# Kernel optimization log

Hardware: AMD Instinct MI355X
Metric: run time of the kernel (lower is better)

## Reference

```python
import jax, jax.numpy as jnp
import numpy as np

B, N, C, H = 2, 2048, 128, 4
C4 = C // 4


def setup_inputs() -> dict:
    key = jax.random.key(0)
    ks = jax.random.split(key, 20)
    s = 0.02
    f = lambda k, sh: (jax.random.normal(k, sh, jnp.float32) * s)
    return {
        'x': jax.random.normal(ks[0], (B, N, C), jnp.float32),
        'A': jax.random.randint(ks[1], (N, N), 0, 2).astype(jnp.int32),
        'q_w1': f(ks[2], (C, C)), 'kv_w1': f(ks[3], (2 * C, C)),
        'proj_w1': f(ks[4], (C, C)), 'proj_b1': jnp.zeros((C,), jnp.float32),
        'q_w2': f(ks[5], (C, C)), 'kv_w2': f(ks[6], (2 * C, C)),
        'proj_w2': f(ks[7], (C, C)), 'proj_b2': jnp.zeros((C,), jnp.float32),
        'cq_w': f(ks[8], (C4, C)), 'cq_b': jnp.zeros((C4,), jnp.float32),
        'ck_w': f(ks[9], (C4, C)), 'ck_b': jnp.zeros((C4,), jnp.float32),
        'cv_w': f(ks[10], (C, C)), 'cv_b': jnp.zeros((C,), jnp.float32),
        'gc_w': f(ks[11], (C, C)), 'gc_b': jnp.zeros((C,), jnp.float32),
    }


def _attn_block(x, A, qw, kvw, pw, pb):
    # Attention._inner_attention + residual; qkv_bias=False, scale=head_dim**-0.5
    b, n, c = x.shape
    hd = c // H
    q = (x @ qw.T).reshape(b, n, H, hd).transpose(0, 2, 1, 3)          # [B,H,N,hd]
    kv = (x @ kvw.T).reshape(b, n, 2, H, hd).transpose(2, 0, 3, 1, 4)  # [2,B,H,N,hd]
    k, v = kv[0], kv[1]
    attn = jnp.einsum('bhnd,bhmd->bhnm', q, k) * (hd ** -0.5)
    attn = jnp.where(A[None, None] > 0, attn, jnp.float32(-9e15))
    attn = jax.nn.softmax(attn, axis=-1)
    out = jnp.einsum('bhnm,bhmd->bhnd', attn, v).transpose(0, 2, 1, 3).reshape(b, n, c)
    return out @ pw.T + pb + x


def _graph_conv(x, cq_w, cq_b, ck_w, ck_b, cv_w, cv_b, gc_w, gc_b):
    # GraphConvolution.forward: conv1d(k=1) QKV, softmax, topk scatter mask, masked softmax, bmm
    b, s, c = x.shape
    xp = x.transpose(0, 2, 1)                                          # [B,C,N]
    query = jnp.einsum('oi,bin->bon', cq_w, xp) + cq_b[:, None]        # [B,C/4,N]
    keyt = (jnp.einsum('oi,bin->bon', ck_w, xp) + ck_b[:, None]).transpose(0, 2, 1)  # [B,N,C/4]
    adj = jax.nn.softmax(jnp.einsum('bnc,bcm->bnm', keyt, query), axis=-1)           # [B,N,N]
    kk = int(s / 3 * 2)                                                # top-2/3 per row
    _, idx = jax.lax.top_k(adj, kk)                                    # [B,N,kk]
    mask = jnp.zeros(adj.shape, bool).at[
        jnp.arange(b)[:, None, None], jnp.arange(s)[None, :, None], idx].set(True)
    adj = jax.nn.softmax(jnp.where(mask, adj, -jnp.inf), axis=-1)
    value = (jnp.einsum('oi,bin->bon', cv_w, xp) + cv_b[:, None]).transpose(0, 2, 1)  # [B,N,C]
    support = value @ gc_w
    return jnp.einsum('bnm,bmc->bnc', adj, support) + gc_b


def reference(x, A, q_w1, kv_w1, proj_w1, proj_b1, q_w2, kv_w2, proj_w2, proj_b2,
              cq_w, cq_b, ck_w, ck_b, cv_w, cv_b, gc_w, gc_b):
    x = _attn_block(x, A, q_w1, kv_w1, proj_w1, proj_b1)
    x = _attn_block(x, A, q_w2, kv_w2, proj_w2, proj_b2)
    return _graph_conv(x, cq_w, cq_b, ck_w, ck_b, cv_w, cv_b, gc_w, gc_b)
```

## Files before the change

### kernel.cpp

```cpp
#include <hip/hip_runtime.h>
#include <hip/hip_bf16.h>
#include <math.h>

#define BB 2
#define NN 2048
#define CC 128
#define HH 4
#define HD 32
#define KK_TOP 1365

typedef __attribute__((ext_vector_type(8))) short v8s;
typedef __attribute__((ext_vector_type(4))) float f32x4;

#define MFMA16(a, b, c) __builtin_amdgcn_mfma_f32_16x16x32_bf16(a, b, c, 0, 0, 0)

__device__ inline float wave_max_f(float v) {
    #pragma unroll
    for (int m = 1; m < 64; m <<= 1) v = fmaxf(v, __shfl_xor(v, m));
    return v;
}
__device__ inline float wave_min_f(float v) {
    #pragma unroll
    for (int m = 1; m < 64; m <<= 1) v = fminf(v, __shfl_xor(v, m));
    return v;
}
__device__ inline float wave_sum_f(float v) {
    #pragma unroll
    for (int m = 1; m < 64; m <<= 1) v += __shfl_xor(v, m);
    return v;
}
__device__ inline unsigned short bf16bits(float x) {
    __hip_bfloat16 h = __float2bfloat16(x);
    return *reinterpret_cast<unsigned short*>(&h);
}

__global__ __launch_bounds__(256) void prep_k(
    const int* __restrict__ A, unsigned* __restrict__ Ab2,
    const float* __restrict__ cv_w, const float* __restrict__ cv_b,
    const float* __restrict__ gc_w, float* __restrict__ MT, float* __restrict__ B2,
    const float* __restrict__ x, short* __restrict__ xb,
    const float* __restrict__ q_w1, const float* __restrict__ kv_w1,
    const float* __restrict__ proj_w1, const float* __restrict__ q_w2,
    const float* __restrict__ kv_w2, const float* __restrict__ proj_w2,
    short* __restrict__ WALLb)
{
    const int bx = blockIdx.x;
    if (bx < 512) {
        const int lane = threadIdx.x & 63;
        const int w = threadIdx.x >> 6;
        const int row = bx * 4 + w;
        const int* rp = A + (size_t)row * 2048;
        for (int i = 0; i < 32; ++i) {
            unsigned long long bal = __ballot(rp[i * 64 + lane] > 0);
            if (lane == 0)  Ab2[(size_t)row * 64 + 2 * i]     = (unsigned)bal;
            if (lane == 32) Ab2[(size_t)row * 64 + 2 * i + 1] = (unsigned)(bal >> 32);
        }
    } else if (bx < 576) {
        const int b2 = bx - 512;
        const int c = b2 * 2 + (threadIdx.x >> 7);
        const int k = threadIdx.x & 127;
        float a = 0.f;
        #pragma unroll 4
        for (int i = 0; i < 128; ++i)
            a += cv_w[(size_t)i * 128 + k] * gc_w[(size_t)i * 128 + c];
        MT[(size_t)c * 128 + k] = a;
        if (b2 == 0 && threadIdx.x < 128) {
            float s = 0.f;
            #pragma unroll 4
            for (int i = 0; i < 128; ++i)
                s += cv_b[i] * gc_w[(size_t)i * 128 + threadIdx.x];
            B2[threadIdx.x] = s;
        }
    } else if (bx < 640) {
        const size_t base = (size_t)(bx - 576) * 8192;
        #pragma unroll 8
        for (int i = 0; i < 32; ++i) {
            size_t e = base + threadIdx.x + i * 256;
            xb[e] = (short)bf16bits(x[e]);
        }
    } else {
        const int base = (bx - 640) * 8192;
        const float* src; int off;
        if (base < 16384)       { src = q_w1;    off = base; }
        else if (base < 49152)  { src = kv_w1;   off = base - 16384; }
        else if (base < 65536)  { src = proj_w1; off = base - 49152; }
        else if (base < 81920)  { src = q_w2;    off = base - 65536; }
        else if (base < 114688) { src = kv_w2;   off = base - 81920; }
        else                    { src = proj_w2; off = base - 114688; }
        short* dst = WALLb + base;
        #pragma unroll 8
        for (int i = 0; i < 32; ++i) {
            int e = threadIdx.x + i * 256;
            dst[e] = (short)bf16bits(src[off + e]);
        }
    }
}

enum { MODE_QKV = 0, MODE_PROJ = 1 };

template <int MODE, bool EMITB>
__global__ __launch_bounds__(256) void mfma_gemm_k(
    const short* __restrict__ Xb, const short* __restrict__ Wb,
    const float* __restrict__ bias, const float* __restrict__ resid,
    short* __restrict__ Qo, short* __restrict__ Ko, short* __restrict__ Vto,
    float* __restrict__ Fo, short* __restrict__ Bo)
{
    const int tid = threadIdx.x;
    const int w = tid >> 6, lane = tid & 63;
    const int g = lane >> 4, c = lane & 15;
    const int m0 = blockIdx.x * 64 + w * 16;
    const int nbase = blockIdx.y * 64;

    v8s af[4];
    #pragma unroll
    for (int kk = 0; kk < 4; ++kk)
        af[kk] = *(const v8s*)(Xb + (size_t)(m0 + c) * 128 + kk * 32 + g * 8);

    for (int nf = 0; nf < 4; ++nf) {
        const int n0 = nbase + nf * 16;
        f32x4 acc = {0.f, 0.f, 0.f, 0.f};
        #pragma unroll
        for (int kk = 0; kk < 4; ++kk) {
            v8s bfr = *(const v8s*)(Wb + (size_t)(n0 + c) * 128 + kk * 32 + g * 8);
            acc = MFMA16(af[kk], bfr, acc);
        }
        const int ccol = n0 + c;
        #pragma unroll
        for (int r = 0; r < 4; ++r) {
            const int m = m0 + 4 * g + r;
            const int b = m >> 11, n = m & 2047;
            if (MODE == MODE_QKV) {
                unsigned short hv = bf16bits(acc[r]);
                if (ccol < 128) {
                    int hh = ccol >> 5, d = ccol & 31;
                    Qo[((size_t)(b * 4 + hh) * 2048 + n) * 32 + d] = (short)hv;
                } else if (ccol < 256) {
                    int c2 = ccol - 128; int hh = c2 >> 5, d = c2 & 31;
                    Ko[((size_t)(b * 4 + hh) * 2048 + n) * 32 + d] = (short)hv;
                } else {
                    int c2 = ccol - 256; int hh = c2 >> 5, d = c2 & 31;
                    Vto[((size_t)(b * 4 + hh) * 32 + d) * 2048 + n] = (short)hv;
                }
            } else {
                float v = acc[r] + bias[ccol] + resid[(size_t)m * 128 + ccol];
                Fo[(size_t)m * 128 + ccol] = v;
                if (EMITB) Bo[(size_t)m * 128 + ccol] = (short)bf16bits(v);
            }
        }
    }
}

__global__ __launch_bounds__(256) void graphmm_k(
    const float* __restrict__ X, const float* __restrict__ cq_w,
    const float* __restrict__ cq_b, const float* __restrict__ ck_w,
    const float* __restrict__ ck_b, const float* __restrict__ MT,
    const float* __restrict__ B2, float* __restrict__ QgT,
    float* __restrict__ Kg, __hip_bfloat16* __restrict__ SUPt)
{
    __shared__ __align__(16) float Xs[64][132];
    __shared__ __align__(16) float Ws[32][132];
    const int tid = threadIdx.x;
    const int m0 = blockIdx.x * 64;
    const int y = blockIdx.y;
    const float* W0   = (y == 0) ? cq_w : (y == 1) ? ck_w : MT;
    const float* bias = (y == 0) ? cq_b : (y == 1) ? ck_b : B2;
    const int n0 = (y < 2) ? 0 : (y - 2) * 32;

    #pragma unroll
    for (int i = 0; i < 32; ++i) {
        int idx = tid + i * 256;
        int row = idx >> 7, col = idx & 127;
        Xs[row][col] = X[(size_t)(m0 + row) * 128 + col];
    }
    #pragma unroll
    for (int i = 0; i < 16; ++i) {
        int idx = tid + i * 256;
        int r = idx >> 7, col = idx & 127;
        Ws[r][col] = W0[(size_t)(n0 + r) * 128 + col];
    }
    __syncthreads();

    const int r = tid >> 4;
    const int c = tid & 15;
    float acc[4][2] = {{0.f, 0.f}, {0.f, 0.f}, {0.f, 0.f}, {0.f, 0.f}};

    #pragma unroll
    for (int k = 0; k < 128; k += 4) {
        float4 w0 = *(const float4*)&Ws[c][k];
        float4 w1 = *(const float4*)&Ws[c + 16][k];
        #pragma unroll
        for (int i = 0; i < 4; ++i) {
            float4 xv = *(const float4*)&Xs[r + 16 * i][k];
            acc[i][0] += xv.x * w0.x + xv.y * w0.y + xv.z * w0.z + xv.w * w0.w;
            acc[i][1] += xv.x * w1.x + xv.y * w1.y + xv.z * w1.z + xv.w * w1.w;
        }
    }

    #pragma unroll
    for (int i = 0; i < 4; ++i) {
        int m = m0 + r + 16 * i;
        int b = m >> 11, n = m & 2047;
        #pragma unroll
        for (int jj = 0; jj < 2; ++jj) {
            int ccol = n0 + c + 16 * jj;
            float v = acc[i][jj];
            if (y == 0) {
                QgT[((size_t)b * 32 + ccol) * 2048 + n] = v + bias[ccol];
            } else if (y == 1) {
                Kg[(size_t)m * 32 + ccol] = v + bias[ccol];
            } else {
                SUPt[((size_t)b * 128 + ccol) * 2048 + n] = __float2bfloat16(v + bias[ccol]);
            }
        }
    }
}

__global__ __launch_bounds__(512, 8) void attn_mfma_k(
    const short* __restrict__ Qb, const short* __restrict__ Kb,
    const short* __restrict__ Vt, const unsigned* __restrict__ Ab2,
    short* __restrict__ Ob)
{
    __shared__ __align__(16) float OLDS[8][64][8];
    __shared__ float lred[8][16];

    const int tid = threadIdx.x;
    const int w = tid >> 6, lane = tid & 63;
    const int g = lane >> 4, c = lane & 15;
    const int bb = 4 * g;
    const int wg = blockIdx.x;
    const int b = wg >> 9, h = (wg >> 7) & 3, r0w = (wg & 127) << 4;
    const int bh = b * 4 + h;

    const v8s qf = *(const v8s*)(Qb + ((size_t)bh * 2048 + r0w + c) * 32 + g * 8);
    const short* Kp = Kb + (size_t)bh * 2048 * 32;
    const short* Vp = Vt + (size_t)bh * 32 * 2048;
    const unsigned* Mrow = Ab2 + (size_t)(r0w + c) * 64;

    f32x4 o0 = {0.f, 0.f, 0.f, 0.f}, o1 = {0.f, 0.f, 0.f, 0.f};
    float lsum = 0.f;
    const float SC2 = 0.25503487f;
    const bool lo = (g < 2);
    const int aA = (32 * (g & 1) + c) * 4;
    const int aB = aA + 64;

    #pragma unroll 2
    for (int t = 0; t < 8; ++t) {
        const int kt = t * 8 + w;
        const int key0 = kt * 32;
        v8s kf0 = *(const v8s*)(Kp + (size_t)(key0 + c) * 32 + g * 8);
        v8s kf1 = *(const v8s*)(Kp + (size_t)(key0 + 16 + c) * 32 + g * 8);
        unsigned mw = Mrow[kt];
        const f32x4 z = {0.f, 0.f, 0.f, 0.f};
        f32x4 s0 = MFMA16(kf0, qf, z);
        f32x4 s1 = MFMA16(kf1, qf, z);

        float p0[4], p1[4];
        #pragma unroll
        for (int r = 0; r < 4; ++r) {
            p0[r] = ((mw >> (bb + r)) & 1u)      ? exp2f(s0[r] * SC2) : 0.f;
            p1[r] = ((mw >> (16 + bb + r)) & 1u) ? exp2f(s1[r] * SC2) : 0.f;
        }
        lsum += p0[0] + p0[1] + p0[2] + p0[3] + p1[0] + p1[1] + p1[2] + p1[3];

        int w00 = (int)bf16bits(p0[0]) | ((int)bf16bits(p0[1]) << 16);
        int w01 = (int)bf16bits(p0[2]) | ((int)bf16bits(p0[3]) << 16);
        int w10 = (int)bf16bits(p1[0]) | ((int)bf16bits(p1[1]) << 16);
        int w11 = (int)bf16bits(p1[2]) | ((int)bf16bits(p1[3]) << 16);

        int e0, e1;
        union { int wv[4]; v8s v; } pf;
        e0 = __builtin_amdgcn_ds_bpermute(aA, w00);
        e1 = __builtin_amdgcn_ds_bpermute(aA, w10);
        pf.wv[0] = lo ? e0 : e1;
        e0 = __builtin_amdgcn_ds_bpermute(aA, w01);
        e1 = __builtin_amdgcn_ds_bpermute(aA, w11);
        pf.wv[1] = lo ? e0 : e1;
        e0 = __builtin_amdgcn_ds_bpermute(aB, w00);
        e1 = __builtin_amdgcn_ds_bpermute(aB, w10);
        pf.wv[2] = lo ? e0 : e1;
        e0 = __builtin_amdgcn_ds_bpermute(aB, w01);
        e1 = __builtin_amdgcn_ds_bpermute(aB, w11);
        pf.wv[3] = lo ? e0 : e1;

        v8s vf0 = *(const v8s*)(Vp + (size_t)c * 2048 + key0 + g * 8);
        v8s vf1 = *(const v8s*)(Vp + (size_t)(16 + c) * 2048 + key0 + g * 8);
        o0 = MFMA16(pf.v, vf0, o0);
        o1 = MFMA16(pf.v, vf1, o1);
    }

    lsum += __shfl_xor(lsum, 16);
    lsum += __shfl_xor(lsum, 32);

    *(f32x4*)&OLDS[w][lane][0] = o0;
    *(f32x4*)&OLDS[w][lane][4] = o1;
    if (lane < 16) lred[w][lane] = lsum;
    __syncthreads();

    if (tid < 64) {
        float iv[4];
        #pragma unroll
        for (int r = 0; r < 4; ++r) {
            float s = lred[0][bb + r];
            #pragma unroll
            for (int ww = 1; ww < 8; ++ww) s += lred[ww][bb + r];
            iv[r] = 1.f / s;
        }
        f32x4 a0 = *(f32x4*)&OLDS[0][lane][0];
        f32x4 a1 = *(f32x4*)&OLDS[0][lane][4];
        #pragma unroll
        for (int ww = 1; ww < 8; ++ww) {
            a0 += *(f32x4*)&OLDS[ww][lane][0];
            a1 += *(f32x4*)&OLDS[ww][lane][4];
        }
        #pragma unroll
        for (int r = 0; r < 4; ++r) {
            size_t base = ((size_t)b * 2048 + r0w + bb + r) * 128 + h * 32;
            Ob[base + c]      = (short)bf16bits(a0[r] * iv[r]);
            Ob[base + 16 + c] = (short)bf16bits(a1[r] * iv[r]);
        }
    }
}

__global__ __launch_bounds__(512, 4) void gadjtopk_k(
    const float* __restrict__ Kg, const float* __restrict__ QgT,
    __hip_bfloat16* __restrict__ ADJb)
{
    __shared__ float kg_s[8][32];
    __shared__ float scores[8][2048];

    const int tid = threadIdx.x;
    const int wg = blockIdx.x;
    const int b = wg >> 8;
    const int r0 = (wg & 255) << 3;

    if (tid < 256) {
        int rr = tid >> 5, d = tid & 31;
        kg_s[rr][d] = Kg[((size_t)b * 2048 + r0 + rr) * 32 + d];
    }
    __syncthreads();

    const float* Qp = QgT + (size_t)b * 32 * 2048;
    float acc[8][4];
    #pragma unroll
    for (int rr = 0; rr < 8; ++rr)
        #pragma unroll
        for (int s = 0; s < 4; ++s) acc[rr][s] = 0.f;

    for (int dd = 0; dd < 32; ++dd) {
        float qv[8];
        #pragma unroll
        for (int rr = 0; rr < 8; ++rr) qv[rr] = kg_s[rr][dd];
        const float* kp = Qp + (size_t)dd * 2048 + tid;
        #pragma unroll
        for (int s = 0; s < 4; ++s) {
            float kv = kp[s * 512];
            #pragma unroll
            for (int rr = 0; rr < 8; ++rr)
                acc[rr][s] = fmaf(qv[rr], kv, acc[rr][s]);
        }
    }
    #pragma unroll
    for (int s = 0; s < 4; ++s) {
        int jj = tid + 512 * s;
        #pragma unroll
        for (int rr = 0; rr < 8; ++rr) scores[rr][jj] = acc[rr][s];
    }
    __syncthreads();

    const int lane = tid & 63, w = tid >> 6;

    float mx = -3.0e38f;
    #pragma unroll
    for (int i = 0; i < 32; ++i) mx = fmaxf(mx, scores[w][lane + i * 64]);
    mx = wave_max_f(mx);

    float sm0 = 0.f;
    #pragma unroll
    for (int i = 0; i < 32; ++i) {
        float p = expf(scores[w][lane + i * 64] - mx);
        scores[w][lane + i * 64] = p;
        sm0 += p;
    }
    sm0 = wave_sum_f(sm0);
    const float ivw = 1.f / sm0;

    unsigned k_[32];
    float mxp = 0.f, mnp = 3.0e38f;
    #pragma unroll
    for (int i = 0; i < 32; ++i) {
        float p = scores[w][lane + i * 64] * ivw;
        k_[i] = __float_as_uint(p);
        mxp = fmaxf(mxp, p);
        mnp = fminf(mnp, p);
    }
    mxp = wave_max_f(mxp);
    mnp = wave_min_f(mnp);

    unsigned thr = __float_as_uint(mnp);
    const unsigned umax = __float_as_uint(mxp);
    const unsigned diff = thr ^ umax;
    if (diff != 0u) {
        const int hb = 31 - __builtin_clz(diff);
        thr = (umax >> (hb + 1)) << (hb + 1);
        for (int bit = hb; bit >= 0; --bit) {
            unsigned cand = thr | (1u << bit);
            int cnt = 0;
            #pragma unroll
            for (int i = 0; i < 32; ++i)
                cnt += (int)__popcll(__ballot(k_[i] >= cand));
            if (cnt == KK_TOP) { thr = cand; break; }
            if (cnt > KK_TOP) thr = cand;
        }
    }

    int gt_c = 0;
    #pragma unroll
    for (int i = 0; i < 32; ++i)
        gt_c += (int)__popcll(__ballot(k_[i] > thr));
    const int need = KK_TOP - gt_c;

    unsigned keepmask = 0u;
    int running = 0;
    const unsigned long long ltmask = (lane == 0) ? 0ull : (~0ull >> (64 - lane));
    #pragma unroll
    for (int i = 0; i < 32; ++i) {
        bool tie = (k_[i] == thr);
        unsigned long long bal = __ballot(tie);
        int before = running + (int)__popcll(bal & ltmask);
        bool keep = (k_[i] > thr) || (tie && before < need);
        running += (int)__popcll(bal);
        if (keep) keepmask |= (1u << i);
    }

    const float LOG2E = 1.4426950408889634f;
    float sm = 0.f;
    #pragma unroll
    for (int i = 0; i < 32; ++i)
        if ((keepmask >> i) & 1u)
            sm += exp2f((__uint_as_float(k_[i]) - mxp) * LOG2E);
    sm = wave_sum_f(sm);
    const float ivs = 1.f / sm;

    __hip_bfloat16* rp = ADJb + (size_t)(b * 2048 + r0 + w) * 2048;
    #pragma unroll
    for (int i = 0; i < 32; ++i) {
        float o = ((keepmask >> i) & 1u)
                    ? exp2f((__uint_as_float(k_[i]) - mxp) * LOG2E) * ivs : 0.f;
        rp[lane + i * 64] = __float2bfloat16(o);
    }
}

__global__ __launch_bounds__(512, 8) void outgemm_mfma_k(
    const short* __restrict__ ADJb, const short* __restrict__ SUPt,
    const float* __restrict__ gcb, float* __restrict__ OUT)
{
    __shared__ __align__(16) float OL[8][64][16];
    const int tid = threadIdx.x;
    const int w = tid >> 6, lane = tid & 63;
    const int g = lane >> 4, c = lane & 15;
    const int r0w = blockIdx.x * 16;
    const int n0 = blockIdx.y * 64;
    const int b = r0w >> 11;
    const short* Bp = SUPt + (size_t)b * 128 * 2048;

    f32x4 acc[4];
    #pragma unroll
    for (int f = 0; f < 4; ++f) acc[f] = (f32x4){0.f, 0.f, 0.f, 0.f};

    #pragma unroll 2
    for (int i = 0; i < 8; ++i) {
        const int k0 = w * 256 + i * 32;
        v8s af = *(const v8s*)(ADJb + (size_t)(r0w + c) * 2048 + k0 + g * 8);
        #pragma unroll
        for (int f = 0; f < 4; ++f) {
            v8s bf_ = *(const v8s*)(Bp + (size_t)(n0 + f * 16 + c) * 2048 + k0 + g * 8);
            acc[f] = MFMA16(af, bf_, acc[f]);
        }
    }

    #pragma unroll
    for (int f = 0; f < 4; ++f) *(f32x4*)&OL[w][lane][f * 4] = acc[f];
    __syncthreads();

    #pragma unroll
    for (int u = 0; u < 2; ++u) {
        int idx = tid + u * 512;
        int ls = idx >> 4, s = idx & 15;
        float v = OL[0][ls][s];
        #pragma unroll
        for (int ww = 1; ww < 8; ++ww) v += OL[ww][ls][s];
        int f = s >> 2, r = s & 3;
        int row = r0w + 4 * (ls >> 4) + r;
        int col = n0 + f * 16 + (ls & 15);
        OUT[(size_t)row * 128 + col] = v + gcb[col];
    }
}

extern "C" void kernel_launch(void* const* d_in, const int* in_sizes, int n_in,
                              void* d_out, int out_size, void* d_ws, size_t ws_size,
                              hipStream_t stream)
{
    const float* x       = (const float*)d_in[0];
    const int*   A       = (const int*)d_in[1];
    const float* q_w1    = (const float*)d_in[2];
    const float* kv_w1   = (const float*)d_in[3];
    const float* proj_w1 = (const float*)d_in[4];
    const float* proj_b1 = (const float*)d_in[5];
    const float* q_w2    = (const float*)d_in[6];
    const float* kv_w2   = (const float*)d_in[7];
    const float* proj_w2 = (const float*)d_in[8];
    const float* proj_b2 = (const float*)d_in[9];
    const float* cq_w    = (const float*)d_in[10];
    const float* cq_b    = (const float*)d_in[11];
    const float* ck_w    = (const float*)d_in[12];
    const float* ck_b    = (const float*)d_in[13];
    const float* cv_w    = (const float*)d_in[14];
    const float* cv_b    = (const float*)d_in[15];
    const float* gc_w    = (const float*)d_in[16];
    const float* gc_b    = (const float*)d_in[17];
    float* out = (float*)d_out;

    char* ws = (char*)d_ws;
    short*          Qb   = (short*)         (ws + 0);
    short*          Kb   = (short*)         (ws + 1048576);
    short*          Vt   = (short*)         (ws + 2097152);
    __hip_bfloat16* ADJb = (__hip_bfloat16*)(ws + 3145728);
    unsigned*       Ab2  = (unsigned*)      (ws + 19922944);
    short*          Ob   = (short*)         (ws + 20447232);
    float*          X1   = (float*)         (ws + 21495808);
    short*          X1b  = (short*)         (ws + 23592960);
    float*          X2   = (float*)         (ws + 24641536);
    float*          QgT  = (float*)         (ws + 26738688);
    float*          Kg   = (float*)         (ws + 27262976);
    __hip_bfloat16* SUPt = (__hip_bfloat16*)(ws + 27787264);
    float*          MT   = (float*)         (ws + 28835840);
    float*          B2   = (float*)         (ws + 28901376);
    short*          xb   = (short*)         (ws + 28901888);
    short*          WALLb= (short*)         (ws + 29950464);

    dim3 blk(256);
    dim3 blk512(512);

    hipLaunchKernelGGL(prep_k, dim3(656), blk, 0, stream,
                       A, Ab2, cv_w, cv_b, gc_w, MT, B2,
                       x, xb, q_w1, kv_w1, proj_w1, q_w2, kv_w2, proj_w2, WALLb);

    hipLaunchKernelGGL((mfma_gemm_k<MODE_QKV, false>), dim3(64, 6), blk, 0, stream,
                       xb, WALLb, nullptr, nullptr, Qb, Kb, Vt, nullptr, nullptr);
    hipLaunchKernelGGL(attn_mfma_k, dim3(1024), blk512, 0, stream,
                       Qb, Kb, Vt, Ab2, Ob);
    hipLaunchKernelGGL((mfma_gemm_k<MODE_PROJ, true>), dim3(64, 2), blk, 0, stream,
                       Ob, WALLb + 49152, proj_b1, x, nullptr, nullptr, nullptr, X1, X1b);

    hipLaunchKernelGGL((mfma_gemm_k<MODE_QKV, false>), dim3(64, 6), blk, 0, stream,
                       X1b, WALLb + 65536, nullptr, nullptr, Qb, Kb, Vt, nullptr, nullptr);
    hipLaunchKernelGGL(attn_mfma_k, dim3(1024), blk512, 0, stream,
                       Qb, Kb, Vt, Ab2, Ob);
    hipLaunchKernelGGL((mfma_gemm_k<MODE_PROJ, false>), dim3(64, 2), blk, 0, stream,
                       Ob, WALLb + 114688, proj_b2, X1, nullptr, nullptr, nullptr, X2, nullptr);

    hipLaunchKernelGGL(graphmm_k, dim3(64, 6), blk, 0, stream,
                       X2, cq_w, cq_b, ck_w, ck_b, MT, B2, QgT, Kg, SUPt);
    hipLaunchKernelGGL(gadjtopk_k, dim3(512), blk512, 0, stream, Kg, QgT, ADJb);
    hipLaunchKernelGGL(outgemm_mfma_k, dim3(256, 2), blk512, 0, stream,
                       (const short*)ADJb, (const short*)SUPt, gc_b, out);
}
```

Measured before the change: 277.9 us.

## Fuse top-k adjacency softmax with output GEMM through shared memory

Merges the top-k masked-softmax kernel and the adjacency-times-support MFMA GEMM into one kernel. The bf16 adjacency rows are written into XOR-swizzled LDS, reusing the scores buffer, instead of a 16 MB global array, and each wave then computes 16 output columns for the block's 8 rows. This removes the global round trip for the adjacency and one launch. In exchange, half of each 16-row MFMA tile is zero padding, and every block re-reads the full support matrix for only 8 rows, so the GEMM is less efficient.

```diff
diff --git a/kernel.cpp b/kernel.cpp
--- a/kernel.cpp
+++ b/kernel.cpp
@@ -2,11 +2,6 @@
 #include <hip/hip_bf16.h>
 #include <math.h>
 
-#define BB 2
-#define NN 2048
-#define CC 128
-#define HH 4
-#define HD 32
 #define KK_TOP 1365
 
 typedef __attribute__((ext_vector_type(8))) short v8s;
@@ -321,12 +316,13 @@
     }
 }
 
-__global__ __launch_bounds__(512, 4) void gadjtopk_k(
+__global__ __launch_bounds__(512, 4) void gadjout_k(
     const float* __restrict__ Kg, const float* __restrict__ QgT,
-    __hip_bfloat16* __restrict__ ADJb)
+    const short* __restrict__ SUPt, const float* __restrict__ gcb,
+    float* __restrict__ OUT)
 {
+    __shared__ __align__(16) float scores[8][2048];
     __shared__ float kg_s[8][32];
-    __shared__ float scores[8][2048];
 
     const int tid = threadIdx.x;
     const int wg = blockIdx.x;
@@ -340,34 +336,37 @@
     __syncthreads();
 
     const float* Qp = QgT + (size_t)b * 32 * 2048;
-    float acc[8][4];
-    #pragma unroll
-    for (int rr = 0; rr < 8; ++rr)
-        #pragma unroll
-        for (int s = 0; s < 4; ++s) acc[rr][s] = 0.f;
-
-    for (int dd = 0; dd < 32; ++dd) {
-        float qv[8];
-        #pragma unroll
-        for (int rr = 0; rr < 8; ++rr) qv[rr] = kg_s[rr][dd];
-        const float* kp = Qp + (size_t)dd * 2048 + tid;
+    {
+        float acc[8][4];
+        #pragma unroll
+        for (int rr = 0; rr < 8; ++rr)
+            #pragma unroll
+            for (int s = 0; s < 4; ++s) acc[rr][s] = 0.f;
+
+        for (int dd = 0; dd < 32; ++dd) {
+            float qv[8];
+            #pragma unroll
+            for (int rr = 0; rr < 8; ++rr) qv[rr] = kg_s[rr][dd];
+            const float* kp = Qp + (size_t)dd * 2048 + tid;
+            #pragma unroll
+            for (int s = 0; s < 4; ++s) {
+                float kv = kp[s * 512];
+                #pragma unroll
+                for (int rr = 0; rr < 8; ++rr)
+                    acc[rr][s] = fmaf(qv[rr], kv, acc[rr][s]);
+            }
+        }
         #pragma unroll
         for (int s = 0; s < 4; ++s) {
-            float kv = kp[s * 512];
+            int jj = tid + 512 * s;
             #pragma unroll
-            for (int rr = 0; rr < 8; ++rr)
-                acc[rr][s] = fmaf(qv[rr], kv, acc[rr][s]);
-        }
-    }
-    #pragma unroll
-    for (int s = 0; s < 4; ++s) {
-        int jj = tid + 512 * s;
-        #pragma unroll
-        for (int rr = 0; rr < 8; ++rr) scores[rr][jj] = acc[rr][s];
+            for (int rr = 0; rr < 8; ++rr) scores[rr][jj] = acc[rr][s];
+        }
     }
     __syncthreads();
 
     const int lane = tid & 63, w = tid >> 6;
+    const int g = lane >> 4, c = lane & 15;
 
     float mx = -3.0e38f;
     #pragma unroll
@@ -395,6 +394,7 @@
     }
     mxp = wave_max_f(mxp);
     mnp = wave_min_f(mnp);
+    __syncthreads();
 
     unsigned thr = __float_as_uint(mnp);
     const unsigned umax = __float_as_uint(mxp);
@@ -441,58 +441,35 @@
     sm = wave_sum_f(sm);
     const float ivs = 1.f / sm;
 
-    __hip_bfloat16* rp = ADJb + (size_t)(b * 2048 + r0 + w) * 2048;
+    unsigned short* adjl = (unsigned short*)&scores[0][0];
+    const int wsw = (w & 7) << 3;
     #pragma unroll
     for (int i = 0; i < 32; ++i) {
         float o = ((keepmask >> i) & 1u)
                     ? exp2f((__uint_as_float(k_[i]) - mxp) * LOG2E) * ivs : 0.f;
-        rp[lane + i * 64] = __float2bfloat16(o);
-    }
-}
-
-__global__ __launch_bounds__(512, 8) void outgemm_mfma_k(
-    const short* __restrict__ ADJb, const short* __restrict__ SUPt,
-    const float* __restrict__ gcb, float* __restrict__ OUT)
-{
-    __shared__ __align__(16) float OL[8][64][16];
-    const int tid = threadIdx.x;
-    const int w = tid >> 6, lane = tid & 63;
-    const int g = lane >> 4, c = lane & 15;
-    const int r0w = blockIdx.x * 16;
-    const int n0 = blockIdx.y * 64;
-    const int b = r0w >> 11;
+        adjl[w * 2048 + ((lane + i * 64) ^ wsw)] = bf16bits(o);
+    }
+    __syncthreads();
+
+    const short* adjs = (const short*)adjl;
     const short* Bp = SUPt + (size_t)b * 128 * 2048;
-
-    f32x4 acc[4];
-    #pragma unroll
-    for (int f = 0; f < 4; ++f) acc[f] = (f32x4){0.f, 0.f, 0.f, 0.f};
-
+    const int csw = (c & 7) << 3;
+    f32x4 oa = {0.f, 0.f, 0.f, 0.f};
+    const v8s zero8 = {0, 0, 0, 0, 0, 0, 0, 0};
     #pragma unroll 2
-    for (int i = 0; i < 8; ++i) {
-        const int k0 = w * 256 + i * 32;
-        v8s af = *(const v8s*)(ADJb + (size_t)(r0w + c) * 2048 + k0 + g * 8);
-        #pragma unroll
-        for (int f = 0; f < 4; ++f) {
-            v8s bf_ = *(const v8s*)(Bp + (size_t)(n0 + f * 16 + c) * 2048 + k0 + g * 8);
-            acc[f] = MFMA16(af, bf_, acc[f]);
-        }
-    }
-
-    #pragma unroll
-    for (int f = 0; f < 4; ++f) *(f32x4*)&OL[w][lane][f * 4] = acc[f];
-    __syncthreads();
-
-    #pragma unroll
-    for (int u = 0; u < 2; ++u) {
-        int idx = tid + u * 512;
-        int ls = idx >> 4, s = idx & 15;
-        float v = OL[0][ls][s];
-        #pragma unroll
-        for (int ww = 1; ww < 8; ++ww) v += OL[ww][ls][s];
-        int f = s >> 2, r = s & 3;
-        int row = r0w + 4 * (ls >> 4) + r;
-        int col = n0 + f * 16 + (ls & 15);
-        OUT[(size_t)row * 128 + col] = v + gcb[col];
+    for (int kf = 0; kf < 64; ++kf) {
+        const int k0 = kf * 32;
+        v8s af2 = (c < 8) ? *(const v8s*)(adjs + (c * 2048 + ((k0 + g * 8) ^ csw)))
+                          : zero8;
+        v8s bf2 = *(const v8s*)(Bp + (size_t)(w * 16 + c) * 2048 + k0 + g * 8);
+        oa = MFMA16(af2, bf2, oa);
+    }
+    if (g < 2) {
+        const int col = w * 16 + c;
+        const float bias = gcb[col];
+        #pragma unroll
+        for (int r = 0; r < 4; ++r)
+            OUT[((size_t)b * 2048 + r0 + 4 * g + r) * 128 + col] = oa[r] + bias;
     }
 }
 
@@ -524,7 +501,6 @@
     short*          Qb   = (short*)         (ws + 0);
     short*          Kb   = (short*)         (ws + 1048576);
     short*          Vt   = (short*)         (ws + 2097152);
-    __hip_bfloat16* ADJb = (__hip_bfloat16*)(ws + 3145728);
     unsigned*       Ab2  = (unsigned*)      (ws + 19922944);
     short*          Ob   = (short*)         (ws + 20447232);
     float*          X1   = (float*)         (ws + 21495808);
@@ -561,7 +537,6 @@
 
     hipLaunchKernelGGL(graphmm_k, dim3(64, 6), blk, 0, stream,
                        X2, cq_w, cq_b, ck_w, ck_b, MT, B2, QgT, Kg, SUPt);
-    hipLaunchKernelGGL(gadjtopk_k, dim3(512), blk512, 0, stream, Kg, QgT, ADJb);
-    hipLaunchKernelGGL(outgemm_mfma_k, dim3(256, 2), blk512, 0, stream,
-                       (const short*)ADJb, (const short*)SUPt, gc_b, out);
-}
+    hipLaunchKernelGGL(gadjout_k, dim3(512), blk512, 0, stream,
+                       Kg, QgT, (const short*)SUPt, gc_b, out);
+}
```

Result: no change. 275.9 us (-0.7%).
